# Performance work log

Measured on AMD Instinct MI355X. Metric: run time of the kernel, lower is better.

## Reference

```python
import jax, jax.numpy as jnp
import numpy as np

EPS = 1e-5

def _ln(x, g, b):
    m = jnp.mean(x, axis=-1, keepdims=True)
    v = jnp.var(x, axis=-1, keepdims=True)
    return (x - m) * jax.lax.rsqrt(v + EPS) * g + b

def _cell(x_t, h_prev, w_rz, b_rz, u_rz, w_h, b_h, u_h, g_rz, be_rz, g_h, be_h):
    # x_t: [B, D], h_prev: [B, H]
    rz = x_t @ w_rz.T + b_rz + h_prev @ u_rz.T          # [B, 2H]
    rz = jax.nn.sigmoid(_ln(rz, g_rz, be_rz))
    H = h_prev.shape[-1]
    r, z = rz[:, :H], rz[:, H:]
    h_tilde = x_t @ w_h.T + b_h + r * (h_prev @ u_h.T)  # [B, H]
    h_tilde = jnp.tanh(_ln(h_tilde, g_h, be_h))
    return (1.0 - z) * h_prev + z * h_tilde

def setup_inputs() -> dict:
    key = jax.random.key(0)
    B, S, D, H, O = 64, 512, 512, 512, 512
    ks = jax.random.split(key, 16)
    s = 0.05  # small init scale for numerical stability
    inp = {
        "x": jax.random.normal(ks[0], (B, S, D), jnp.float32),
        "fc_w": s * jax.random.normal(ks[1], (O, H), jnp.float32),
        "fc_b": jnp.zeros((O,), jnp.float32),
    }
    for li, base in ((0, 2), (1, 8)):
        p = f"l{li}_"
        din = D if li == 0 else H
        inp[p + "w_rz"] = s * jax.random.normal(ks[base], (2 * H, din), jnp.float32)
        inp[p + "b_rz"] = jnp.zeros((2 * H,), jnp.float32)
        inp[p + "u_rz"] = s * jax.random.normal(ks[base + 1], (2 * H, H), jnp.float32)
        inp[p + "w_h"] = s * jax.random.normal(ks[base + 2], (H, din), jnp.float32)
        inp[p + "b_h"] = jnp.zeros((H,), jnp.float32)
        inp[p + "u_h"] = s * jax.random.normal(ks[base + 3], (H, H), jnp.float32)
        inp[p + "ln_rz_g"] = jnp.ones((2 * H,), jnp.float32)
        inp[p + "ln_rz_b"] = jnp.zeros((2 * H,), jnp.float32)
        inp[p + "ln_h_g"] = jnp.ones((H,), jnp.float32)
        inp[p + "ln_h_b"] = jnp.zeros((H,), jnp.float32)
    return inp

def reference(x,
              l0_w_rz, l0_b_rz, l0_u_rz, l0_w_h, l0_b_h, l0_u_h,
              l0_ln_rz_g, l0_ln_rz_b, l0_ln_h_g, l0_ln_h_b,
              l1_w_rz, l1_b_rz, l1_u_rz, l1_w_h, l1_b_h, l1_u_h,
              l1_ln_rz_g, l1_ln_rz_b, l1_ln_h_g, l1_ln_h_b,
              fc_w, fc_b):
    B, S, D = x.shape
    H = l0_u_h.shape[0]
    p0 = (l0_w_rz, l0_b_rz, l0_u_rz, l0_w_h, l0_b_h, l0_u_h,
          l0_ln_rz_g, l0_ln_rz_b, l0_ln_h_g, l0_ln_h_b)
    p1 = (l1_w_rz, l1_b_rz, l1_u_rz, l1_w_h, l1_b_h, l1_u_h,
          l1_ln_rz_g, l1_ln_rz_b, l1_ln_h_g, l1_ln_h_b)

    def step(carry, x_t):
        h0, h1 = carry
        h0 = _cell(x_t, h0, *p0)   # dropout=0 between layers
        h1 = _cell(h0, h1, *p1)
        return (h0, h1), h1

    h_init = (jnp.zeros((B, H), x.dtype), jnp.zeros((B, H), x.dtype))
    (h0, h1), ys = jax.lax.scan(step, h_init, jnp.swapaxes(x, 0, 1))  # ys: [S,B,H]
    out = jnp.swapaxes(ys, 0, 1)                 # [B,S,H]
    logits = out @ fc_w.T + fc_b                 # [B,S,O]
    hidden = jnp.stack([h0, h1])                 # [2,B,H]
    return logits, hidden
```

## Files before the change

### kernel.cpp

```cpp
#include <hip/hip_runtime.h>
#include <stdint.h>

typedef _Float16 f16;
typedef _Float16 f16x8 __attribute__((ext_vector_type(8)));
typedef float f32x4 __attribute__((ext_vector_type(4)));

#define LN_EPS 1e-5f

#define AT_LD(p)   __hip_atomic_load((p), __ATOMIC_RELAXED, __HIP_MEMORY_SCOPE_AGENT)
#define AT_ST(p,v) __hip_atomic_store((p), (v), __ATOMIC_RELAXED, __HIP_MEMORY_SCOPE_AGENT)
#define VM_DRAIN() asm volatile("s_waitcnt vmcnt(0)" ::: "memory")

__device__ __forceinline__ void bar_slot(uint32_t* slots, int g, uint32_t e,
                                         int tid) {
  VM_DRAIN();
  __syncthreads();
  if (tid == 0) AT_ST(&slots[g * 16], e);
  if (tid < 12) {
    while (AT_LD(&slots[tid * 16]) < e) __builtin_amdgcn_s_sleep(1);
  }
  __syncthreads();
}

__device__ __forceinline__ float fast_sigmoid(float a) {
  return __builtin_amdgcn_rcpf(1.f + __expf(-a));
}
__device__ __forceinline__ float fast_tanh(float a) {
  float x = fminf(fmaxf(a, -15.f), 15.f);
  return 1.f - 2.f * __builtin_amdgcn_rcpf(1.f + __expf(2.f * x));
}

__global__ __launch_bounds__(512, 2) void scan_fused(
    const f16* __restrict__ X0,
    const f16* __restrict__ W1,
    const f16* __restrict__ U0,
    const f16* __restrict__ U1,
    const float* __restrict__ bias1,
    const float* __restrict__ g_rz0, const float* __restrict__ b_rz0,
    const float* __restrict__ g_h0,  const float* __restrict__ b_h0,
    const float* __restrict__ g_rz1, const float* __restrict__ b_rz1,
    const float* __restrict__ g_h1,  const float* __restrict__ b_h1,
    f16* __restrict__ h_all0,
    f16* __restrict__ h_all1,
    float* __restrict__ h32_0, float* __restrict__ h32_1,
    float* __restrict__ pre,
    uint32_t* __restrict__ bars)
{
  const int blk   = blockIdx.x;
  const int chunk = blk & 7;
  const int g     = blk >> 3;
  const int layer = chunk >> 2;
  const int rows0 = (chunk & 3) * 16;
  const int tid  = threadIdx.x;
  const int wid  = tid >> 6;
  const int lane = tid & 63;
  const int quad = lane >> 4;
  const int l16  = lane & 15;
  const int col  = g * 128 + wid * 16 + l16;
  const bool rz_cols = (g * 128 + wid * 16) < 1024;
  const int myrow = (wid == 0) ? g : ((wid == 1 && g < 4) ? 12 + g : -1);

  __shared__ f16 Ash[16][1048];
  __shared__ float lnrg[1024], lnrb[1024], lnhg[512], lnhb[512];

  {
    const float* srg = layer ? g_rz1 : g_rz0;
    const float* srb = layer ? b_rz1 : b_rz0;
    const float* shg = layer ? g_h1  : g_h0;
    const float* shb = layer ? b_h1  : b_h0;
    for (int i = tid; i < 1024; i += 512) { lnrg[i] = srg[i]; lnrb[i] = srb[i]; }
    if (tid < 512) { lnhg[tid] = shg[tid]; lnhb[tid] = shb[tid]; }
    f16* az = &Ash[0][0];
    for (int i = tid; i < 16 * 1048; i += 512) az[i] = (f16)0.f;
  }

  f16x8 ufw[16], ufu[16];
  if (layer == 0) {
#pragma unroll
    for (int kk = 0; kk < 16; ++kk)
      ufu[kk] = *(const f16x8*)(U0 + (size_t)col * 512 + kk * 32 + quad * 8);
  } else {
#pragma unroll
    for (int kk = 0; kk < 16; ++kk) {
      ufw[kk] = *(const f16x8*)(W1 + (size_t)col * 512 + kk * 32 + quad * 8);
      ufu[kk] = *(const f16x8*)(U1 + (size_t)col * 512 + kk * 32 + quad * 8);
    }
  }
  const float bval = layer ? bias1[col] : 0.f;

  uint32_t* slots1 = bars + (size_t)chunk * 512;
  uint32_t* slots2 = slots1 + 256;
  uint32_t* peer2  = bars + (size_t)(chunk & 3) * 512 + 256;

  float hreg[8];
#pragma unroll
  for (int i = 0; i < 8; ++i) hreg[i] = 0.f;

  const size_t prerow0 = (size_t)layer * 64 + rows0;
  f16* h_out = layer ? h_all1 : h_all0;

  float xzc[4] = {0.f, 0.f, 0.f, 0.f};
  f16 xpfc[8];
  if (layer == 0) {
    if (rz_cols) {
      const size_t xb = ((size_t)rows0 + quad * 4) * 1536 + col;
#pragma unroll
      for (int rr = 0; rr < 4; ++rr) xzc[rr] = (float)X0[xb + (size_t)rr * 1536];
    }
    if (myrow >= 0) {
      const size_t xh = ((size_t)rows0 + myrow) * 1536 + 1024 + lane;
#pragma unroll
      for (int i = 0; i < 8; ++i) xpfc[i] = X0[xh + (size_t)i * 64];
    }
  }

  for (int t = 0; t < 512; ++t) {
    if (layer == 1) {
      if (tid < 12) {
        while (AT_LD(&peer2[tid * 16]) < (uint32_t)(t + 1))
          __builtin_amdgcn_s_sleep(1);
      }
      __syncthreads();
    }
    {
      const int r  = tid >> 5;
      const int k0 = (tid & 31) * 16;
      if (layer == 1) {
        const uint64_t* s0 =
            (const uint64_t*)(h_all0 + ((size_t)t * 64 + rows0 + r) * 512 + k0);
        uint64_t a0 = AT_LD(s0), a1 = AT_LD(s0 + 1),
                 a2 = AT_LD(s0 + 2), a3 = AT_LD(s0 + 3);
        uint64_t* d0 = (uint64_t*)&Ash[r][k0];
        d0[0] = a0; d0[1] = a1; d0[2] = a2; d0[3] = a3;
        if (t > 0) {
          const uint64_t* s1 =
              (const uint64_t*)(h_all1 + ((size_t)(t - 1) * 64 + rows0 + r) * 512 + k0);
          uint64_t b0 = AT_LD(s1), b1 = AT_LD(s1 + 1),
                   b2 = AT_LD(s1 + 2), b3 = AT_LD(s1 + 3);
          uint64_t* d1 = (uint64_t*)&Ash[r][512 + k0];
          d1[0] = b0; d1[1] = b1; d1[2] = b2; d1[3] = b3;
        }
      } else if (t > 0) {
        const uint64_t* s0 =
            (const uint64_t*)(h_all0 + ((size_t)(t - 1) * 64 + rows0 + r) * 512 + k0);
        uint64_t a0 = AT_LD(s0), a1 = AT_LD(s0 + 1),
                 a2 = AT_LD(s0 + 2), a3 = AT_LD(s0 + 3);
        uint64_t* d0 = (uint64_t*)&Ash[r][k0];
        d0[0] = a0; d0[1] = a1; d0[2] = a2; d0[3] = a3;
      }
    }
    __syncthreads();

    f32x4 accw = (f32x4){0.f, 0.f, 0.f, 0.f};
    f32x4 accu = (f32x4){0.f, 0.f, 0.f, 0.f};
    if (layer == 0) {
#pragma unroll
      for (int kk = 0; kk < 8; ++kk) {
        f16x8 af = *(const f16x8*)&Ash[l16][kk * 32 + quad * 8];
        accw = __builtin_amdgcn_mfma_f32_16x16x32_f16(af, ufu[kk], accw, 0, 0, 0);
      }
#pragma unroll
      for (int kk = 8; kk < 16; ++kk) {
        f16x8 af = *(const f16x8*)&Ash[l16][kk * 32 + quad * 8];
        accu = __builtin_amdgcn_mfma_f32_16x16x32_f16(af, ufu[kk], accu, 0, 0, 0);
      }
    } else {
      accw = (f32x4){bval, bval, bval, bval};
#pragma unroll
      for (int kk = 0; kk < 16; ++kk) {
        f16x8 af = *(const f16x8*)&Ash[l16][kk * 32 + quad * 8];
        accw = __builtin_amdgcn_mfma_f32_16x16x32_f16(af, ufw[kk], accw, 0, 0, 0);
      }
#pragma unroll
      for (int kk = 0; kk < 16; ++kk) {
        f16x8 af = *(const f16x8*)&Ash[l16][512 + kk * 32 + quad * 8];
        accu = __builtin_amdgcn_mfma_f32_16x16x32_f16(af, ufu[kk], accu, 0, 0, 0);
      }
    }

    const int buf = t & 1;
    {
      float* prow0 = pre + ((size_t)buf * 128 + prerow0 + quad * 4) * 2048;
      if (layer == 0) {
#pragma unroll
        for (int rr = 0; rr < 4; ++rr)
          AT_ST(&prow0[(size_t)rr * 2048 + col], accw[rr] + accu[rr] + xzc[rr]);
      } else if (rz_cols) {
#pragma unroll
        for (int rr = 0; rr < 4; ++rr)
          AT_ST(&prow0[(size_t)rr * 2048 + col], accw[rr] + accu[rr]);
      } else {
#pragma unroll
        for (int rr = 0; rr < 4; ++rr) {
          AT_ST(&prow0[(size_t)rr * 2048 + col],       accu[rr]);
          AT_ST(&prow0[(size_t)rr * 2048 + col + 512], accw[rr]);
        }
      }
    }

    bar_slot(slots1, g, (uint32_t)(t + 1), tid);

    float xzn[4] = {0.f, 0.f, 0.f, 0.f};
    f16 xpfn[8];
    if (layer == 0) {
      const int tn = (t < 511) ? t + 1 : 511;
      if (rz_cols) {
        const size_t xb = ((size_t)tn * 64 + rows0 + quad * 4) * 1536 + col;
#pragma unroll
        for (int rr = 0; rr < 4; ++rr) xzn[rr] = (float)X0[xb + (size_t)rr * 1536];
      }
      if (myrow >= 0) {
        const size_t xh = ((size_t)tn * 64 + rows0 + myrow) * 1536 + 1024 + lane;
#pragma unroll
        for (int i = 0; i < 8; ++i) xpfn[i] = X0[xh + (size_t)i * 64];
      }
    }

    if (myrow >= 0) {
      const int brow = rows0 + myrow;
      float* prow =
          pre + ((size_t)buf * 128 + (size_t)layer * 64 + brow) * 2048;
      float v[16], hu[8], xh[8];
#pragma unroll
      for (int i = 0; i < 16; ++i) v[i] = AT_LD(&prow[i * 64 + lane]);
#pragma unroll
      for (int i = 0; i < 8; ++i)  hu[i] = AT_LD(&prow[1024 + i * 64 + lane]);
      if (layer) {
#pragma unroll
        for (int i = 0; i < 8; ++i) xh[i] = AT_LD(&prow[1536 + i * 64 + lane]);
      }
      float s1 = 0.f, s2 = 0.f;
#pragma unroll
      for (int i = 0; i < 16; ++i) { s1 += v[i]; s2 += v[i] * v[i]; }
#pragma unroll
      for (int off = 1; off < 64; off <<= 1) {
        s1 += __shfl_xor(s1, off); s2 += __shfl_xor(s2, off);
      }
      float m    = s1 * (1.f / 1024.f);
      float var  = s2 * (1.f / 1024.f) - m * m;
      float rstd = rsqrtf(var + LN_EPS);
      float rg[8], zg[8];
#pragma unroll
      for (int i = 0; i < 16; ++i) {
        int n = i * 64 + lane;
        float a = (v[i] - m) * rstd * lnrg[n] + lnrb[n];
        float s = fast_sigmoid(a);
        if (i < 8) rg[i] = s; else zg[i - 8] = s;
      }
      float ht[8];
      float u1 = 0.f, u2 = 0.f;
#pragma unroll
      for (int i = 0; i < 8; ++i) {
        float xv = layer ? xh[i] : (float)xpfc[i];
        float hv = xv + rg[i] * hu[i];
        ht[i] = hv; u1 += hv; u2 += hv * hv;
      }
#pragma unroll
      for (int off = 1; off < 64; off <<= 1) {
        u1 += __shfl_xor(u1, off); u2 += __shfl_xor(u2, off);
      }
      float m2    = u1 * (1.f / 512.f);
      float var2  = u2 * (1.f / 512.f) - m2 * m2;
      float rstd2 = rsqrtf(var2 + LN_EPS);
#pragma unroll
      for (int i = 0; i < 8; ++i) {
        int n = i * 64 + lane;
        float a  = (ht[i] - m2) * rstd2 * lnhg[n] + lnhb[n];
        float th = fast_tanh(a);
        float hn = (1.f - zg[i]) * hreg[i] + zg[i] * th;
        hreg[i] = hn;
        union { f16 h; uint16_t u; } cv; cv.h = (f16)hn;
        AT_ST((uint16_t*)&h_out[((size_t)t * 64 + brow) * 512 + n], cv.u);
      }
    }

    bar_slot(slots2, g, (uint32_t)(t + 1), tid);

    if (layer == 0) {
#pragma unroll
      for (int rr = 0; rr < 4; ++rr) xzc[rr] = xzn[rr];
#pragma unroll
      for (int i = 0; i < 8; ++i) xpfc[i] = xpfn[i];
    }
  }

  if (myrow >= 0) {
    float* hdst = layer ? h32_1 : h32_0;
    const int brow = rows0 + myrow;
#pragma unroll
    for (int i = 0; i < 8; ++i)
      hdst[(size_t)brow * 512 + i * 64 + lane] = hreg[i];
  }
}

__global__ void gemm_k512(const f16* __restrict__ A, const f16* __restrict__ W,
                          const float* __restrict__ bias, void* __restrict__ out,
                          int N, int mode)
{
  __shared__ f16 As[128][56];
  __shared__ f16 Bs[128][56];
  const int tid = threadIdx.x;
  const int wid = tid >> 6, lane = tid & 63, quad = lane >> 4, l16 = lane & 15;
  const int wm = wid & 1, wn = wid >> 1;
  const int rb = blockIdx.y * 128, cb = blockIdx.x * 128;
  f32x4 acc[4][4];
#pragma unroll
  for (int i = 0; i < 4; ++i)
#pragma unroll
    for (int j = 0; j < 4; ++j) acc[i][j] = (f32x4){0.f, 0.f, 0.f, 0.f};
  const int srow = tid >> 1;
  const int skh  = (tid & 1) * 16;
  for (int kk = 0; kk < 16; ++kk) {
    __syncthreads();
    {
      const f16* a = A + (size_t)(rb + srow) * 512 + kk * 32 + skh;
      *(f16x8*)&As[srow][skh]     = *(const f16x8*)(a);
      *(f16x8*)&As[srow][skh + 8] = *(const f16x8*)(a + 8);
      const f16* b = W + (size_t)(cb + srow) * 512 + kk * 32 + skh;
      *(f16x8*)&Bs[srow][skh]     = *(const f16x8*)(b);
      *(f16x8*)&Bs[srow][skh + 8] = *(const f16x8*)(b + 8);
    }
    __syncthreads();
    f16x8 af[4], bf[4];
#pragma unroll
    for (int mt = 0; mt < 4; ++mt) af[mt] = *(const f16x8*)&As[wm * 64 + mt * 16 + l16][quad * 8];
#pragma unroll
    for (int nt = 0; nt < 4; ++nt) bf[nt] = *(const f16x8*)&Bs[wn * 64 + nt * 16 + l16][quad * 8];
#pragma unroll
    for (int mt = 0; mt < 4; ++mt)
#pragma unroll
      for (int nt = 0; nt < 4; ++nt)
        acc[mt][nt] = __builtin_amdgcn_mfma_f32_16x16x32_f16(af[mt], bf[nt], acc[mt][nt], 0, 0, 0);
  }
#pragma unroll
  for (int mt = 0; mt < 4; ++mt) {
#pragma unroll
    for (int nt = 0; nt < 4; ++nt) {
#pragma unroll
      for (int rr = 0; rr < 4; ++rr) {
        int grow = rb + wm * 64 + mt * 16 + quad * 4 + rr;
        int gcol = cb + wn * 64 + nt * 16 + l16;
        float vv = acc[mt][nt][rr] + bias[gcol];
        if (mode == 0) {
          ((f16*)out)[(size_t)grow * N + gcol] = (f16)vv;
        } else {
          int b = grow & 63, tt = grow >> 6;
          ((float*)out)[((size_t)b * 512 + tt) * 512 + gcol] = vv;
        }
      }
    }
  }
}

__global__ void prep_kernel(
    const float* __restrict__ x, const float* __restrict__ fc_w,
    const float* __restrict__ w_rz0, const float* __restrict__ b_rz0,
    const float* __restrict__ u_rz0, const float* __restrict__ w_h0,
    const float* __restrict__ b_h0,  const float* __restrict__ u_h0,
    const float* __restrict__ w_rz1, const float* __restrict__ b_rz1,
    const float* __restrict__ u_rz1, const float* __restrict__ w_h1,
    const float* __restrict__ b_h1,  const float* __restrict__ u_h1,
    f16* x16, f16* wcat0, f16* ucat0, f16* wcat1, f16* ucat1, f16* fcw16,
    float* bias0, float* bias1, float* h32_0, float* h32_1, uint32_t* bars)
{
  const int stride = gridDim.x * blockDim.x;
  const int gid = blockIdx.x * blockDim.x + threadIdx.x;
  for (int i = gid; i < 16777216; i += stride) {
    int k = i & 511, b = (i >> 9) & 63, t = i >> 15;
    x16[i] = (f16)x[(((size_t)b << 9) + t) * 512 + k];
  }
  for (int i = gid; i < 786432; i += stride) {
    int n = i >> 9, k = i & 511;
    float a0 = (n < 1024) ? w_rz0[(size_t)n * 512 + k] : w_h0[(size_t)(n - 1024) * 512 + k];
    float c0 = (n < 1024) ? u_rz0[(size_t)n * 512 + k] : u_h0[(size_t)(n - 1024) * 512 + k];
    float a1 = (n < 1024) ? w_rz1[(size_t)n * 512 + k] : w_h1[(size_t)(n - 1024) * 512 + k];
    float c1 = (n < 1024) ? u_rz1[(size_t)n * 512 + k] : u_h1[(size_t)(n - 1024) * 512 + k];
    wcat0[i] = (f16)a0; ucat0[i] = (f16)c0; wcat1[i] = (f16)a1; ucat1[i] = (f16)c1;
  }
  for (int i = gid; i < 262144; i += stride) fcw16[i] = (f16)fc_w[i];
  for (int i = gid; i < 1536; i += stride) {
    bias0[i] = (i < 1024) ? b_rz0[i] : b_h0[i - 1024];
    bias1[i] = (i < 1024) ? b_rz1[i] : b_h1[i - 1024];
  }
  for (int i = gid; i < 32768; i += stride) { h32_0[i] = 0.f; h32_1[i] = 0.f; }
  for (int i = gid; i < 4096; i += stride) bars[i] = 0u;
}

__global__ void tail_kernel(const float* __restrict__ h32_0,
                            const float* __restrict__ h32_1,
                            float* __restrict__ out)
{
  int i = blockIdx.x * blockDim.x + threadIdx.x;
  if (i < 32768)      out[16777216 + i] = h32_0[i];
  else if (i < 65536) out[16777216 + i] = h32_1[i - 32768];
}

extern "C" void kernel_launch(void* const* d_in, const int* in_sizes, int n_in,
                              void* d_out, int out_size, void* d_ws, size_t ws_size,
                              hipStream_t stream)
{
  const float* x      = (const float*)d_in[0];
  const float* fc_w   = (const float*)d_in[1];
  const float* fc_b   = (const float*)d_in[2];
  const float* l0_w_rz = (const float*)d_in[3];
  const float* l0_b_rz = (const float*)d_in[4];
  const float* l0_u_rz = (const float*)d_in[5];
  const float* l0_w_h  = (const float*)d_in[6];
  const float* l0_b_h  = (const float*)d_in[7];
  const float* l0_u_h  = (const float*)d_in[8];
  const float* l0_g_rz = (const float*)d_in[9];
  const float* l0_be_rz= (const float*)d_in[10];
  const float* l0_g_h  = (const float*)d_in[11];
  const float* l0_be_h = (const float*)d_in[12];
  const float* l1_w_rz = (const float*)d_in[13];
  const float* l1_b_rz = (const float*)d_in[14];
  const float* l1_u_rz = (const float*)d_in[15];
  const float* l1_w_h  = (const float*)d_in[16];
  const float* l1_b_h  = (const float*)d_in[17];
  const float* l1_u_h  = (const float*)d_in[18];
  const float* l1_g_rz = (const float*)d_in[19];
  const float* l1_be_rz= (const float*)d_in[20];
  const float* l1_g_h  = (const float*)d_in[21];
  const float* l1_be_h = (const float*)d_in[22];

  char* ws = (char*)d_ws;
  size_t off = 0;
  auto alloc = [&](size_t bytes) {
    size_t o = off; off += (bytes + 255) & ~(size_t)255; return o;
  };
  f16*   X      = (f16*)  (ws + alloc((size_t)512 * 64 * 1536 * 2));
  f16*   x16    = (f16*)  (ws + alloc((size_t)512 * 64 * 512 * 2));
  f16*   h_all0 = (f16*)  (ws + alloc((size_t)512 * 64 * 512 * 2));
  f16*   h_all1 = (f16*)  (ws + alloc((size_t)512 * 64 * 512 * 2));
  f16*   wcat0  = (f16*)  (ws + alloc((size_t)1536 * 512 * 2));
  f16*   ucat0  = (f16*)  (ws + alloc((size_t)1536 * 512 * 2));
  f16*   wcat1  = (f16*)  (ws + alloc((size_t)1536 * 512 * 2));
  f16*   ucat1  = (f16*)  (ws + alloc((size_t)1536 * 512 * 2));
  f16*   fcw16  = (f16*)  (ws + alloc((size_t)512 * 512 * 2));
  float* bias0  = (float*)(ws + alloc((size_t)1536 * 4));
  float* bias1  = (float*)(ws + alloc((size_t)1536 * 4));
  float* h32_0  = (float*)(ws + alloc((size_t)64 * 512 * 4));
  float* h32_1  = (float*)(ws + alloc((size_t)64 * 512 * 4));
  float* pre    = (float*)(ws + alloc((size_t)2 * 128 * 2048 * 4));
  uint32_t* bars= (uint32_t*)(ws + alloc((size_t)4096 * 4));

  prep_kernel<<<dim3(2048), dim3(256), 0, stream>>>(
      x, fc_w, l0_w_rz, l0_b_rz, l0_u_rz, l0_w_h, l0_b_h, l0_u_h,
      l1_w_rz, l1_b_rz, l1_u_rz, l1_w_h, l1_b_h, l1_u_h,
      x16, wcat0, ucat0, wcat1, ucat1, fcw16, bias0, bias1,
      h32_0, h32_1, bars);

  gemm_k512<<<dim3(12, 256), dim3(256), 0, stream>>>(x16, wcat0, bias0, X, 1536, 0);

  scan_fused<<<dim3(96), dim3(512), 0, stream>>>(
      X, wcat1, ucat0, ucat1, bias1,
      l0_g_rz, l0_be_rz, l0_g_h, l0_be_h,
      l1_g_rz, l1_be_rz, l1_g_h, l1_be_h,
      h_all0, h_all1, h32_0, h32_1, pre, bars);

  gemm_k512<<<dim3(4, 256), dim3(256), 0, stream>>>(h_all1, fcw16, fc_b, d_out, 512, 1);
  tail_kernel<<<dim3(256), dim3(256), 0, stream>>>(h32_0, h32_1, (float*)d_out);
}
```

Measured before the change: 4.040 ms.

## Replace group barriers with per-row producer/owner flags in fused GRU scan

```diff
diff --git a/kernel.cpp b/kernel.cpp
--- a/kernel.cpp
+++ b/kernel.cpp
@@ -10,17 +10,6 @@
 #define AT_LD(p)   __hip_atomic_load((p), __ATOMIC_RELAXED, __HIP_MEMORY_SCOPE_AGENT)
 #define AT_ST(p,v) __hip_atomic_store((p), (v), __ATOMIC_RELAXED, __HIP_MEMORY_SCOPE_AGENT)
 #define VM_DRAIN() asm volatile("s_waitcnt vmcnt(0)" ::: "memory")
-
-__device__ __forceinline__ void bar_slot(uint32_t* slots, int g, uint32_t e,
-                                         int tid) {
-  VM_DRAIN();
-  __syncthreads();
-  if (tid == 0) AT_ST(&slots[g * 16], e);
-  if (tid < 12) {
-    while (AT_LD(&slots[tid * 16]) < e) __builtin_amdgcn_s_sleep(1);
-  }
-  __syncthreads();
-}
 
 __device__ __forceinline__ float fast_sigmoid(float a) {
   return __builtin_amdgcn_rcpf(1.f + __expf(-a));
@@ -88,9 +77,9 @@
   }
   const float bval = layer ? bias1[col] : 0.f;
 
-  uint32_t* slots1 = bars + (size_t)chunk * 512;
-  uint32_t* slots2 = slots1 + 256;
-  uint32_t* peer2  = bars + (size_t)(chunk & 3) * 512 + 256;
+  uint32_t* prodf  = bars + (size_t)chunk * 2048;
+  uint32_t* ownf   = prodf + 1024;
+  uint32_t* l0ownf = bars + (size_t)(chunk & 3) * 2048 + 1024;
 
   float hreg[8];
 #pragma unroll
@@ -101,6 +90,8 @@
 
   float xzc[4] = {0.f, 0.f, 0.f, 0.f};
   f16 xpfc[8];
+  float xzn[4];
+  f16 xpfn[8];
   if (layer == 0) {
     if (rz_cols) {
       const size_t xb = ((size_t)rows0 + quad * 4) * 1536 + col;
@@ -115,66 +106,70 @@
   }
 
   for (int t = 0; t < 512; ++t) {
-    if (layer == 1) {
-      if (tid < 12) {
-        while (AT_LD(&peer2[tid * 16]) < (uint32_t)(t + 1))
-          __builtin_amdgcn_s_sleep(1);
+    if (t > 0) {
+      if (tid < 16) {
+        while (AT_LD(&ownf[tid * 16]) < (uint32_t)t) { }
       }
       __syncthreads();
-    }
-    {
-      const int r  = tid >> 5;
-      const int k0 = (tid & 31) * 16;
-      if (layer == 1) {
+      if (layer == 0) {
+#pragma unroll
+        for (int rr = 0; rr < 4; ++rr) xzc[rr] = xzn[rr];
+#pragma unroll
+        for (int i = 0; i < 8; ++i) xpfc[i] = xpfn[i];
+      }
+      {
+        const int r  = tid >> 5;
+        const int k0 = (tid & 31) * 16;
+        const f16* hsrc = layer ? h_all1 : h_all0;
+        const uint64_t* s0 =
+            (const uint64_t*)(hsrc + ((size_t)(t - 1) * 64 + rows0 + r) * 512 + k0);
+        uint64_t a0 = AT_LD(s0), a1 = AT_LD(s0 + 1),
+                 a2 = AT_LD(s0 + 2), a3 = AT_LD(s0 + 3);
+        uint64_t* d0 = (uint64_t*)&Ash[r][(layer ? 512 : 0) + k0];
+        d0[0] = a0; d0[1] = a1; d0[2] = a2; d0[3] = a3;
+      }
+    }
+    __syncthreads();
+
+    f32x4 accw = (f32x4){0.f, 0.f, 0.f, 0.f};
+    f32x4 accu = (f32x4){0.f, 0.f, 0.f, 0.f};
+    if (layer == 0) {
+#pragma unroll
+      for (int kk = 0; kk < 8; ++kk) {
+        f16x8 af = *(const f16x8*)&Ash[l16][kk * 32 + quad * 8];
+        accw = __builtin_amdgcn_mfma_f32_16x16x32_f16(af, ufu[kk], accw, 0, 0, 0);
+      }
+#pragma unroll
+      for (int kk = 8; kk < 16; ++kk) {
+        f16x8 af = *(const f16x8*)&Ash[l16][kk * 32 + quad * 8];
+        accu = __builtin_amdgcn_mfma_f32_16x16x32_f16(af, ufu[kk], accu, 0, 0, 0);
+      }
+    } else {
+      accw = (f32x4){bval, bval, bval, bval};
+#pragma unroll
+      for (int kk = 0; kk < 16; ++kk) {
+        f16x8 af = *(const f16x8*)&Ash[l16][512 + kk * 32 + quad * 8];
+        accu = __builtin_amdgcn_mfma_f32_16x16x32_f16(af, ufu[kk], accu, 0, 0, 0);
+      }
+      if (tid < 16) {
+        while (AT_LD(&l0ownf[tid * 16]) < (uint32_t)(t + 1)) { }
+      }
+      __syncthreads();
+      {
+        const int r  = tid >> 5;
+        const int k0 = (tid & 31) * 16;
         const uint64_t* s0 =
             (const uint64_t*)(h_all0 + ((size_t)t * 64 + rows0 + r) * 512 + k0);
         uint64_t a0 = AT_LD(s0), a1 = AT_LD(s0 + 1),
                  a2 = AT_LD(s0 + 2), a3 = AT_LD(s0 + 3);
         uint64_t* d0 = (uint64_t*)&Ash[r][k0];
         d0[0] = a0; d0[1] = a1; d0[2] = a2; d0[3] = a3;
-        if (t > 0) {
-          const uint64_t* s1 =
-              (const uint64_t*)(h_all1 + ((size_t)(t - 1) * 64 + rows0 + r) * 512 + k0);
-          uint64_t b0 = AT_LD(s1), b1 = AT_LD(s1 + 1),
-                   b2 = AT_LD(s1 + 2), b3 = AT_LD(s1 + 3);
-          uint64_t* d1 = (uint64_t*)&Ash[r][512 + k0];
-          d1[0] = b0; d1[1] = b1; d1[2] = b2; d1[3] = b3;
-        }
-      } else if (t > 0) {
-        const uint64_t* s0 =
-            (const uint64_t*)(h_all0 + ((size_t)(t - 1) * 64 + rows0 + r) * 512 + k0);
-        uint64_t a0 = AT_LD(s0), a1 = AT_LD(s0 + 1),
-                 a2 = AT_LD(s0 + 2), a3 = AT_LD(s0 + 3);
-        uint64_t* d0 = (uint64_t*)&Ash[r][k0];
-        d0[0] = a0; d0[1] = a1; d0[2] = a2; d0[3] = a3;
-      }
-    }
-    __syncthreads();
-
-    f32x4 accw = (f32x4){0.f, 0.f, 0.f, 0.f};
-    f32x4 accu = (f32x4){0.f, 0.f, 0.f, 0.f};
-    if (layer == 0) {
-#pragma unroll
-      for (int kk = 0; kk < 8; ++kk) {
-        f16x8 af = *(const f16x8*)&Ash[l16][kk * 32 + quad * 8];
-        accw = __builtin_amdgcn_mfma_f32_16x16x32_f16(af, ufu[kk], accw, 0, 0, 0);
-      }
-#pragma unroll
-      for (int kk = 8; kk < 16; ++kk) {
-        f16x8 af = *(const f16x8*)&Ash[l16][kk * 32 + quad * 8];
-        accu = __builtin_amdgcn_mfma_f32_16x16x32_f16(af, ufu[kk], accu, 0, 0, 0);
-      }
-    } else {
-      accw = (f32x4){bval, bval, bval, bval};
+      }
+      __syncthreads();
 #pragma unroll
       for (int kk = 0; kk < 16; ++kk) {
         f16x8 af = *(const f16x8*)&Ash[l16][kk * 32 + quad * 8];
         accw = __builtin_amdgcn_mfma_f32_16x16x32_f16(af, ufw[kk], accw, 0, 0, 0);
-      }
-#pragma unroll
-      for (int kk = 0; kk < 16; ++kk) {
-        f16x8 af = *(const f16x8*)&Ash[l16][512 + kk * 32 + quad * 8];
-        accu = __builtin_amdgcn_mfma_f32_16x16x32_f16(af, ufu[kk], accu, 0, 0, 0);
       }
     }
 
@@ -197,26 +192,16 @@
         }
       }
     }
-
-    bar_slot(slots1, g, (uint32_t)(t + 1), tid);
-
-    float xzn[4] = {0.f, 0.f, 0.f, 0.f};
-    f16 xpfn[8];
-    if (layer == 0) {
-      const int tn = (t < 511) ? t + 1 : 511;
-      if (rz_cols) {
-        const size_t xb = ((size_t)tn * 64 + rows0 + quad * 4) * 1536 + col;
-#pragma unroll
-        for (int rr = 0; rr < 4; ++rr) xzn[rr] = (float)X0[xb + (size_t)rr * 1536];
-      }
-      if (myrow >= 0) {
-        const size_t xh = ((size_t)tn * 64 + rows0 + myrow) * 1536 + 1024 + lane;
-#pragma unroll
-        for (int i = 0; i < 8; ++i) xpfn[i] = X0[xh + (size_t)i * 64];
-      }
-    }
+    VM_DRAIN();
+    __syncthreads();
+    if (tid == 0) AT_ST(&prodf[g * 16], (uint32_t)(t + 1));
 
     if (myrow >= 0) {
+      for (;;) {
+        bool ok = (lane < 12 && lane != g)
+                      ? (AT_LD(&prodf[lane * 16]) >= (uint32_t)(t + 1)) : true;
+        if (__all(ok)) break;
+      }
       const int brow = rows0 + myrow;
       float* prow =
           pre + ((size_t)buf * 128 + (size_t)layer * 64 + brow) * 2048;
@@ -272,15 +257,25 @@
         union { f16 h; uint16_t u; } cv; cv.h = (f16)hn;
         AT_ST((uint16_t*)&h_out[((size_t)t * 64 + brow) * 512 + n], cv.u);
       }
-    }
-
-    bar_slot(slots2, g, (uint32_t)(t + 1), tid);
+      VM_DRAIN();
+      if (lane == 0) AT_ST(&ownf[myrow * 16], (uint32_t)(t + 1));
+    }
 
     if (layer == 0) {
-#pragma unroll
-      for (int rr = 0; rr < 4; ++rr) xzc[rr] = xzn[rr];
-#pragma unroll
-      for (int i = 0; i < 8; ++i) xpfc[i] = xpfn[i];
+      const int tn = (t < 511) ? t + 1 : 511;
+      if (rz_cols) {
+        const size_t xb = ((size_t)tn * 64 + rows0 + quad * 4) * 1536 + col;
+#pragma unroll
+        for (int rr = 0; rr < 4; ++rr) xzn[rr] = (float)X0[xb + (size_t)rr * 1536];
+      } else {
+#pragma unroll
+        for (int rr = 0; rr < 4; ++rr) xzn[rr] = 0.f;
+      }
+      if (myrow >= 0) {
+        const size_t xh = ((size_t)tn * 64 + rows0 + myrow) * 1536 + 1024 + lane;
+#pragma unroll
+        for (int i = 0; i < 8; ++i) xpfn[i] = X0[xh + (size_t)i * 64];
+      }
     }
   }
 
@@ -383,7 +378,7 @@
     bias1[i] = (i < 1024) ? b_rz1[i] : b_h1[i - 1024];
   }
   for (int i = gid; i < 32768; i += stride) { h32_0[i] = 0.f; h32_1[i] = 0.f; }
-  for (int i = gid; i < 4096; i += stride) bars[i] = 0u;
+  for (int i = gid; i < 16384; i += stride) bars[i] = 0u;
 }
 
 __global__ void tail_kernel(const float* __restrict__ h32_0,
@@ -442,7 +437,7 @@
   float* h32_0  = (float*)(ws + alloc((size_t)64 * 512 * 4));
   float* h32_1  = (float*)(ws + alloc((size_t)64 * 512 * 4));
   float* pre    = (float*)(ws + alloc((size_t)2 * 128 * 2048 * 4));
-  uint32_t* bars= (uint32_t*)(ws + alloc((size_t)4096 * 4));
+  uint32_t* bars= (uint32_t*)(ws + alloc((size_t)16384 * 4));
 
   prep_kernel<<<dim3(2048), dim3(256), 0, stream>>>(
       x, fc_w, l0_w_rz, l0_b_rz, l0_u_rz, l0_w_h, l0_b_h, l0_u_h,
```

Result: slower. 4.239 ms (+4.9%).
